# Kernel tuning notes

Measured on AMD Instinct MI355X. Metric: run time of the kernel, lower is better.

## Reference

```python
import jax, jax.numpy as jnp
import numpy as np

B, S, D, H = 2, 2048, 1024, 16
HD = D // H               # head_dim = input_size / num_heads
STEPS = 1                 # update_steps_max extra Hopfield update steps
LN_EPS = 1e-5
SCALING = 1.0 / np.sqrt(HD)  # beta = 1/sqrt(head_dim)


def layernorm(x, g, b):
    m = x.mean(-1, keepdims=True)
    v = ((x - m) ** 2).mean(-1, keepdims=True)
    return (x - m) * jax.lax.rsqrt(v + LN_EPS) * g + b


def setup_inputs() -> dict:
    key = jax.random.key(0)
    ks = jax.random.split(key, 9)
    s = 0.02
    f32 = jnp.float32
    return {
        "data": jax.random.normal(ks[0], (B, S, D), f32),
        # affine LayerNorm params (stored / state / projection patterns)
        "g_k": jnp.ones((D,), f32), "b_k": jnp.zeros((D,), f32),
        "g_q": jnp.ones((D,), f32), "b_q": jnp.zeros((D,), f32),
        "g_v": jnp.ones((D,), f32), "b_v": jnp.zeros((D,), f32),
        # in-projections (q/k/v) and out-projection of HopfieldCore
        "Wq": jax.random.normal(ks[1], (D, D), f32) * s, "bq": jnp.zeros((D,), f32),
        "Wk": jax.random.normal(ks[2], (D, D), f32) * s, "bk": jnp.zeros((D,), f32),
        "Wv": jax.random.normal(ks[3], (D, D), f32) * s, "bv": jnp.zeros((D,), f32),
        "Wo": jax.random.normal(ks[4], (D, D), f32) * s, "bo": jnp.zeros((D,), f32),
    }


def reference(data, g_k, b_k, g_q, b_q, g_v, b_v,
              Wq, bq, Wk, bk, Wv, bv, Wo, bo):
    # single input tensor used as stored / state / projection pattern
    xk = layernorm(data, g_k, b_k)   # stored pattern  -> keys
    xq = layernorm(data, g_q, b_q)   # state pattern   -> queries
    xv = layernorm(data, g_v, b_v)   # pattern proj    -> values

    split = lambda t: t.reshape(B, S, H, HD).transpose(0, 2, 1, 3)  # [B,H,S,HD]
    q = split(xq @ Wq + bq)
    k = split(xk @ Wk + bk)
    v = split(xv @ Wv + bv)

    def assoc(q):  # xi = softmax(beta * q K^T)
        return jax.nn.softmax(
            jnp.einsum('bhqd,bhkd->bhqk', q, k) * SCALING, axis=-1)

    xi = assoc(q)
    for _ in range(STEPS):           # iterative Hopfield update: q <- xi K
        q = jnp.einsum('bhqk,bhkd->bhqd', xi, k)
        xi = assoc(q)

    out = jnp.einsum('bhqk,bhkd->bhqd', xi, v)        # retrieve with values
    out = out.transpose(0, 2, 1, 3).reshape(B, S, D)  # merge heads
    return out @ Wo + bo
```

## Files before the change

### kernel.cpp

```cpp
#include <hip/hip_runtime.h>
#include <hip/hip_bf16.h>

#define B_  2
#define S_  2048
#define D_  1024
#define H_  16
#define HD_ 64
#define M_  4096


typedef __attribute__((ext_vector_type(8))) short short8;
typedef __attribute__((ext_vector_type(4))) float f32x4;
typedef __attribute__((ext_vector_type(2))) float f32x2;
typedef __attribute__((ext_vector_type(16))) float f32x16;

#define CE_ 0.1803368801111204f

typedef __attribute__((address_space(1))) const unsigned GU;
typedef __attribute__((address_space(3))) unsigned LU;
static __device__ __forceinline__ void glds16(const void* g, void* l){
  __builtin_amdgcn_global_load_lds((GU*)g, (LU*)l, 16, 0, 0);
}

static __device__ __forceinline__ unsigned short f2bfc(float f){
  union{float f; unsigned u;} c; c.f = f;
  return (unsigned short)((c.u + 0x8000u) >> 16);
}
static __device__ __forceinline__ unsigned pk2bf(float a, float b){
  union{float f; unsigned u;} ca, cb; ca.f=a; cb.f=b;
  return __builtin_amdgcn_perm(cb.u + 0x8000u, ca.u + 0x8000u, 0x07060302u);
}
static __device__ __forceinline__ unsigned pk2bft(float a, float b){
  union{float f; unsigned u;} ca, cb; ca.f=a; cb.f=b;
  return __builtin_amdgcn_perm(cb.u, ca.u, 0x07060302u);
}
static __device__ __forceinline__ short8 mk8(unsigned x0, unsigned x1,
                                             unsigned x2, unsigned x3){
  union{ unsigned u[4]; short8 s; } t;
  t.u[0]=x0; t.u[1]=x1; t.u[2]=x2; t.u[3]=x3; return t.s;
}
static __device__ __forceinline__ void plswap(unsigned &x, unsigned &y){
  auto r = __builtin_amdgcn_permlane32_swap(x, y, false, false);
  x = (unsigned)r[0]; y = (unsigned)r[1];
}
static __device__ __forceinline__ short8 conv8a(const f32x16& v, float iv){
  unsigned a0 = pk2bf(v[0]*iv, v[1]*iv);
  unsigned a1 = pk2bf(v[2]*iv, v[3]*iv);
  unsigned b0 = pk2bf(v[4]*iv, v[5]*iv);
  unsigned b1 = pk2bf(v[6]*iv, v[7]*iv);
  plswap(a0,b0); plswap(a1,b1);
  return mk8(a0,a1,b0,b1);
}
static __device__ __forceinline__ short8 conv8b(const f32x16& v, float iv){
  unsigned a0 = pk2bf(v[8]*iv,  v[9]*iv);
  unsigned a1 = pk2bf(v[10]*iv, v[11]*iv);
  unsigned b0 = pk2bf(v[12]*iv, v[13]*iv);
  unsigned b1 = pk2bf(v[14]*iv, v[15]*iv);
  plswap(a0,b0); plswap(a1,b1);
  return mk8(a0,a1,b0,b1);
}

__global__ __launch_bounds__(256) void prep_kernel(
  const float* __restrict__ data,
  const float* __restrict__ Wq, const float* __restrict__ Wk,
  const float* __restrict__ Wv, const float* __restrict__ Wo,
  const float* __restrict__ gq, const float* __restrict__ gk, const float* __restrict__ gv,
  const float* __restrict__ blq, const float* __restrict__ blk, const float* __restrict__ blv,
  const float* __restrict__ bpq, const float* __restrict__ bpk, const float* __restrict__ bpv,
  unsigned short* __restrict__ WT, unsigned short* __restrict__ xhat,
  float* __restrict__ bf)
{
  __shared__ unsigned short tile[64][72];
  __shared__ float red[4][64];
  int bid = blockIdx.x, t = threadIdx.x;
  if (bid < 1024){
    int z = bid >> 8, rem = bid & 255;
    int k0 = (rem>>4)*64, n0 = (rem&15)*64;
    const float* W = (z==0)?Wq:(z==1)?Wk:(z==2)?Wv:Wo;
    const float* g = (z==0)?gq:(z==1)?gk:(z==2)?gv:(const float*)0;
    unsigned short* out = WT + ((size_t)z<<20);
    {
      int kr = t>>2, c16 = (t&3)*16;
      float gs = g ? g[k0+kr]*((z==0)?CE_:1.0f) : 1.0f;
      const float* src = W + (size_t)(k0+kr)*D_ + n0 + c16;
      float4 w0 = *(const float4*)(src);
      float4 w1 = *(const float4*)(src+4);
      float4 w2 = *(const float4*)(src+8);
      float4 w3 = *(const float4*)(src+12);
      unsigned* tp = (unsigned*)&tile[kr][c16];
      tp[0]=pk2bf(w0.x*gs,w0.y*gs); tp[1]=pk2bf(w0.z*gs,w0.w*gs);
      tp[2]=pk2bf(w1.x*gs,w1.y*gs); tp[3]=pk2bf(w1.z*gs,w1.w*gs);
      tp[4]=pk2bf(w2.x*gs,w2.y*gs); tp[5]=pk2bf(w2.z*gs,w2.w*gs);
      tp[6]=pk2bf(w3.x*gs,w3.y*gs); tp[7]=pk2bf(w3.z*gs,w3.w*gs);
    }
    __syncthreads();
    {
      int nr = t>>2, kc = (t&3)*16;
      union { uint4 v[2]; unsigned short u[16]; } st;
      #pragma unroll
      for (int i=0;i<16;i++) st.u[i] = tile[kc+i][nr];
      unsigned short* dst = out + (size_t)(n0+nr)*D_ + k0 + kc;
      *(uint4*)(dst)     = st.v[0];
      *(uint4*)(dst + 8) = st.v[1];
    }
  } else if (bid < 2048){
    int row = (bid-1024)*4 + (t>>6);
    int l = t & 63;
    const float4* xr = (const float4*)(data + (size_t)row*D_);
    float4 v[4];
    float s = 0.f, ss = 0.f;
    #pragma unroll
    for (int i=0;i<4;i++){
      v[i] = xr[l + 64*i];
      s  += v[i].x+v[i].y+v[i].z+v[i].w;
      ss += v[i].x*v[i].x+v[i].y*v[i].y+v[i].z*v[i].z+v[i].w*v[i].w;
    }
    #pragma unroll
    for (int m=1;m<64;m<<=1){ s += __shfl_xor(s, m, 64); ss += __shfl_xor(ss, m, 64); }
    float me = s*(1.0f/D_);
    float var = ss*(1.0f/D_) - me*me;
    float rs = rsqrtf(var + 1e-5f);
    float nm = -me*rs;
    unsigned short* xo = xhat + (size_t)row*D_;
    #pragma unroll
    for (int i=0;i<4;i++){
      uint2 pk;
      pk.x = pk2bf(fmaf(v[i].x,rs,nm), fmaf(v[i].y,rs,nm));
      pk.y = pk2bf(fmaf(v[i].z,rs,nm), fmaf(v[i].w,rs,nm));
      *(uint2*)(xo + 4*l + 256*i) = pk;
    }
  } else {
    int idx = bid - 2048;
    int z = idx >> 4, xb = idx & 15;
    const float* W  = (z==0)?Wq:(z==1)?Wk:Wv;
    const float* bl = (z==0)?blq:(z==1)?blk:blv;
    const float* bp = (z==0)?bpq:(z==1)?bpk:bpv;
    int nl = t & 63, kg = t >> 6;
    int n = xb*64 + nl;
    float acc = 0.f;
    for (int k = kg*256; k < (kg+1)*256; k++)
      acc += bl[k] * W[(size_t)k*D_ + n];
    red[kg][nl] = acc;
    __syncthreads();
    if (t < 64){
      int nn = xb*64 + t;
      float v = red[0][t]+red[1][t]+red[2][t]+red[3][t] + bp[nn];
      bf[z*D_ + nn] = (z==0) ? v*CE_ : v;
    }
  }
}

__global__ __launch_bounds__(256) void gemm_qkv(
  const unsigned short* __restrict__ xhat,
  const unsigned short* __restrict__ WT,
  const float* __restrict__ biasf,
  unsigned short* __restrict__ qv, unsigned short* __restrict__ kb,
  unsigned short* __restrict__ kT, unsigned short* __restrict__ vT)
{
  int z = blockIdx.z;
  const unsigned short* Bt = WT + ((size_t)z<<20);
  const float* bias = biasf + z*D_;
  unsigned short* oN = (z==0)?qv:(z==1)?kb:(unsigned short*)0;
  unsigned short* oT = (z==0)?(unsigned short*)0:(z==1)?kT:vT;

  __shared__ __align__(16) unsigned short As[128*32];
  __shared__ __align__(16) unsigned short Bs[128*32];
  int tid = threadIdx.x, w = tid>>6, l = tid&63;
  int m0 = blockIdx.x*128, n0 = blockIdx.y*128;
  int wr = (w>>1)*64, wc = (w&1)*64;
  int lr = l&15, qd = l>>4;

  const unsigned short* gA = xhat + (size_t)(m0 + w*32 + (l>>2))*D_ + (l&3)*8;
  const unsigned short* gB = Bt   + (size_t)(n0 + w*32 + (l>>2))*D_ + (l&3)*8;
  unsigned short* lA0 = &As[(w*32)*32];
  unsigned short* lA1 = &As[(w*32+16)*32];
  unsigned short* lB0 = &Bs[(w*32)*32];
  unsigned short* lB1 = &Bs[(w*32+16)*32];

  const f32x4 fz = {0.f,0.f,0.f,0.f};
  f32x4 acc[4][4];
  #pragma unroll
  for (int i=0;i<4;i++)
    #pragma unroll
    for (int j=0;j<4;j++) acc[i][j] = fz;

  for (int kk=0; kk<D_; kk+=32){
    __syncthreads();
    glds16(gA + kk,                 lA0);
    glds16(gA + kk + (size_t)16*D_, lA1);
    glds16(gB + kk,                 lB0);
    glds16(gB + kk + (size_t)16*D_, lB1);
    __syncthreads();
    short8 af[4], bfr[4];
    #pragma unroll
    for (int i=0;i<4;i++) af[i]  = *(const short8*)(As + (wr + i*16 + lr)*32 + qd*8);
    #pragma unroll
    for (int j=0;j<4;j++) bfr[j] = *(const short8*)(Bs + (wc + j*16 + lr)*32 + qd*8);
    #pragma unroll
    for (int i=0;i<4;i++)
      #pragma unroll
      for (int j=0;j<4;j++)
        acc[i][j] = __builtin_amdgcn_mfma_f32_16x16x32_bf16(af[i], bfr[j], acc[i][j], 0, 0, 0);
  }

  #pragma unroll
  for (int j=0;j<4;j++){
    int n = n0 + wc + j*16 + lr;
    float bias_n = bias[n];
    #pragma unroll
    for (int i=0;i<4;i++){
      int mb = m0 + wr + i*16 + qd*4;
      float v0 = acc[i][j][0] + bias_n;
      float v1 = acc[i][j][1] + bias_n;
      float v2 = acc[i][j][2] + bias_n;
      float v3 = acc[i][j][3] + bias_n;
      if (oN){
        oN[(size_t)(mb+0)*D_ + n] = f2bfc(v0);
        oN[(size_t)(mb+1)*D_ + n] = f2bfc(v1);
        oN[(size_t)(mb+2)*D_ + n] = f2bfc(v2);
        oN[(size_t)(mb+3)*D_ + n] = f2bfc(v3);
      }
      if (oT){
        int bb = mb >> 11, sI = mb & (S_-1);
        int hh = n >> 6,  dd = n & 63;
        uint2 pk; pk.x = pk2bf(v0, v1); pk.y = pk2bf(v2, v3);
        *(uint2*)(oT + (size_t)((bb*H_ + hh)*HD_ + dd)*S_ + sI) = pk;
      }
    }
  }
}

__global__ __launch_bounds__(256) void gemm_out(
  const unsigned short* __restrict__ A,
  const unsigned short* __restrict__ Bt,
  const float* __restrict__ bo,
  float* __restrict__ Cf)
{
  __shared__ __align__(16) unsigned short As[128*32];
  __shared__ __align__(16) unsigned short Bs[128*32];
  int tid = threadIdx.x, w = tid>>6, l = tid&63;
  int m0 = blockIdx.x*128, n0 = blockIdx.y*128;
  int wr = (w>>1)*64, wc = (w&1)*64;
  int lr = l&15, qd = l>>4;

  const unsigned short* gA = A  + (size_t)(m0 + w*32 + (l>>2))*D_ + (l&3)*8;
  const unsigned short* gB = Bt + (size_t)(n0 + w*32 + (l>>2))*D_ + (l&3)*8;
  unsigned short* lA0 = &As[(w*32)*32];
  unsigned short* lA1 = &As[(w*32+16)*32];
  unsigned short* lB0 = &Bs[(w*32)*32];
  unsigned short* lB1 = &Bs[(w*32+16)*32];

  const f32x4 fz = {0.f,0.f,0.f,0.f};
  f32x4 acc[4][4];
  #pragma unroll
  for (int i=0;i<4;i++)
    #pragma unroll
    for (int j=0;j<4;j++) acc[i][j] = fz;

  for (int kk=0; kk<D_; kk+=32){
    __syncthreads();
    glds16(gA + kk,                 lA0);
    glds16(gA + kk + (size_t)16*D_, lA1);
    glds16(gB + kk,                 lB0);
    glds16(gB + kk + (size_t)16*D_, lB1);
    __syncthreads();
    short8 af[4], bfr[4];
    #pragma unroll
    for (int i=0;i<4;i++) af[i]  = *(const short8*)(As + (wr + i*16 + lr)*32 + qd*8);
    #pragma unroll
    for (int j=0;j<4;j++) bfr[j] = *(const short8*)(Bs + (wc + j*16 + lr)*32 + qd*8);
    #pragma unroll
    for (int i=0;i<4;i++)
      #pragma unroll
      for (int j=0;j<4;j++)
        acc[i][j] = __builtin_amdgcn_mfma_f32_16x16x32_bf16(af[i], bfr[j], acc[i][j], 0, 0, 0);
  }

  #pragma unroll
  for (int j=0;j<4;j++){
    int n = n0 + wc + j*16 + lr;
    float bias_n = bo[n];
    #pragma unroll
    for (int i=0;i<4;i++){
      int mb = m0 + wr + i*16 + qd*4;
      Cf[(size_t)(mb+0)*D_ + n] = acc[i][j][0] + bias_n;
      Cf[(size_t)(mb+1)*D_ + n] = acc[i][j][1] + bias_n;
      Cf[(size_t)(mb+2)*D_ + n] = acc[i][j][2] + bias_n;
      Cf[(size_t)(mb+3)*D_ + n] = acc[i][j][3] + bias_n;
    }
  }
}

__global__ __launch_bounds__(256, 4) void attn_fused(
  unsigned short* __restrict__ QO,
  const unsigned short* __restrict__ K,
  const unsigned short* __restrict__ KT,
  const unsigned short* __restrict__ VT)
{
  int qt = blockIdx.x;
  int h  = blockIdx.y;
  int b  = qt >> 5;
  int bh = b*H_ + h;
  int tid = threadIdx.x, w = tid>>6, l = tid&63;
  int wq = w & 1, wk = w >> 1;
  int lq = l & 31, hi = l >> 5;
  int swzr = (lq & 7) << 3;

  __shared__ __align__(16) unsigned short smem[17408];

  const f32x16 fz16 = {0.f,0.f,0.f,0.f,0.f,0.f,0.f,0.f,
                       0.f,0.f,0.f,0.f,0.f,0.f,0.f,0.f};

  const unsigned short* Qb = QO + (size_t)(qt*64 + wq*32 + lq)*D_ + h*64;
  short8 qf[4];
  #pragma unroll
  for (int d=0; d<4; d++) qf[d] = *(const short8*)(Qb + d*16 + hi*8);

  const unsigned short* Khead = K + (size_t)(b*S_)*D_ + h*64;
  const unsigned short* Vh0 = KT + (size_t)bh*HD_*S_;
  const unsigned short* Vh1 = VT + (size_t)bh*HD_*S_;

  int seg0 = w*2;
  int lr8 = l>>3;
  int swzs = ((l&7)*8) ^ (lr8*8);
  const unsigned short* gKs  = Khead + (size_t)(seg0*8 + lr8)*D_ + swzs;
  const unsigned short* gV0s = Vh0 + (size_t)(seg0*8 + lr8)*S_ + swzs;
  const unsigned short* gV1s = Vh1 + (size_t)(seg0*8 + lr8)*S_ + swzs;
  int dK0 = seg0*512 + l*8;
  int dV0 = 4096 + seg0*512 + l*8;

  glds16(gKs,         smem + dK0);
  glds16(gKs + 8*D_,  smem + dK0 + 512);
  glds16(gV0s,        smem + dV0);
  glds16(gV0s + 8*S_, smem + dV0 + 512);
  __syncthreads();

  #pragma unroll 1
  for (int phase=0; phase<2; phase++){
    f32x16 oacc[2]; oacc[0]=fz16; oacc[1]=fz16;
    f32x2 dq = {0.f,0.f};

    #pragma unroll 1
    for (int ss=0; ss<32; ss++){
      int t = phase*32 + ss;
      if (t < 63){
        int tn = t + 1;
        int tt = tn & 31;
        unsigned short* bb = smem + ((tn&1) ? 8192 : 0);
        const unsigned short* gk = gKs + (size_t)tt*64*D_;
        const unsigned short* gv = ((tn >= 32) ? gV1s : gV0s) + tt*64;
        glds16(gk,         bb + dK0);
        glds16(gk + 8*D_,  bb + dK0 + 512);
        glds16(gv,         bb + dV0);
        glds16(gv + 8*S_,  bb + dV0 + 512);
      }
      __builtin_amdgcn_sched_barrier(0);

      const unsigned short* sKc = smem + ((t&1) ? 8192 : 0);
      const unsigned short* sVc = sKc + 4096;

      f32x16 sc = fz16;
      __builtin_amdgcn_s_setprio(1);
      #pragma unroll
      for (int d4=0; d4<4; d4++){
        short8 ka = *(const short8*)(sKc + (size_t)(wk*32 + lq)*64 + ((d4*16 + hi*8) ^ swzr));
        sc = __builtin_amdgcn_mfma_f32_32x32x16_bf16(ka, qf[d4], sc, 0,0,0);
      }
      __builtin_amdgcn_s_setprio(0);

      #pragma unroll
      for (int i=0;i<16;i++) sc[i] = __builtin_amdgcn_exp2f(sc[i]);
      #pragma unroll
      for (int i=0;i<16;i+=2) dq += (f32x2){sc[i], sc[i+1]};

      short8 pf[2];
      {
        unsigned a0,a1,b0,b1;
        a0=pk2bft(sc[0],sc[1]);   a1=pk2bft(sc[2],sc[3]);
        b0=pk2bft(sc[4],sc[5]);   b1=pk2bft(sc[6],sc[7]);
        plswap(a0,b0); plswap(a1,b1);
        pf[0] = mk8(a0,a1,b0,b1);
        a0=pk2bft(sc[8],sc[9]);   a1=pk2bft(sc[10],sc[11]);
        b0=pk2bft(sc[12],sc[13]); b1=pk2bft(sc[14],sc[15]);
        plswap(a0,b0); plswap(a1,b1);
        pf[1] = mk8(a0,a1,b0,b1);
      }

      __builtin_amdgcn_s_setprio(1);
      #pragma unroll
      for (int dr=0; dr<2; dr++){
        #pragma unroll
        for (int ks=0; ks<2; ks++){
          short8 va = *(const short8*)(sVc + (size_t)(dr*32 + lq)*64 + ((wk*32 + ks*16 + hi*8) ^ swzr));
          oacc[dr] = __builtin_amdgcn_mfma_f32_32x32x16_bf16(va, pf[ks], oacc[dr], 0,0,0);
        }
      }
      __builtin_amdgcn_s_setprio(0);

      __syncthreads();
    }

    float den = dq.x + dq.y;
    den += __shfl_xor(den, 32, 64);

    float* fb  = (float*)(smem + 8192);
    float* dnp = (float*)(smem + 16384);
    if (wk==1){
      #pragma unroll
      for (int dr=0; dr<2; dr++)
        #pragma unroll
        for (int g=0; g<16; g++)
          fb[wq*2048 + (dr*16+g)*64 + l] = oacc[dr][g];
      dnp[wq*64 + l] = den;
    }
    __syncthreads();
    if (wk==0){
      #pragma unroll
      for (int dr=0; dr<2; dr++)
        #pragma unroll
        for (int g=0; g<16; g++)
          oacc[dr][g] += fb[wq*2048 + (dr*16+g)*64 + l];
      den += dnp[wq*64 + l];
      if (phase==0){
        float iv = CE_ * __builtin_amdgcn_rcpf(den);
        qf[0] = conv8a(oacc[0], iv);
        qf[1] = conv8b(oacc[0], iv);
        qf[2] = conv8a(oacc[1], iv);
        qf[3] = conv8b(oacc[1], iv);
        unsigned short* qsh = smem + 8192 + wq*6144;
        #pragma unroll
        for (int d=0; d<4; d++)
          *(short8*)(qsh + d*512 + l*8) = qf[d];
      } else {
        float iv = __builtin_amdgcn_rcpf(den);
        unsigned short* Ob = QO + (size_t)(qt*64 + wq*32 + lq)*D_ + h*64 + hi*4;
        #pragma unroll
        for (int g=0; g<4; g++){
          uint2 pk;
          pk.x = pk2bf(oacc[0][4*g+0]*iv, oacc[0][4*g+1]*iv);
          pk.y = pk2bf(oacc[0][4*g+2]*iv, oacc[0][4*g+3]*iv);
          *(uint2*)(Ob + g*8) = pk;
          pk.x = pk2bf(oacc[1][4*g+0]*iv, oacc[1][4*g+1]*iv);
          pk.y = pk2bf(oacc[1][4*g+2]*iv, oacc[1][4*g+3]*iv);
          *(uint2*)(Ob + 32 + g*8) = pk;
        }
      }
    }
    __syncthreads();
    if (phase==0 && wk==1){
      unsigned short* qsh = smem + 8192 + wq*6144;
      #pragma unroll
      for (int d=0; d<4; d++)
        qf[d] = *(const short8*)(qsh + d*512 + l*8);
    }
    __syncthreads();
  }
}

extern "C" void kernel_launch(void* const* d_in, const int* in_sizes, int n_in,
                              void* d_out, int out_size, void* d_ws, size_t ws_size,
                              hipStream_t stream){
  const float* data = (const float*)d_in[0];
  const float* g_k  = (const float*)d_in[1];
  const float* b_k  = (const float*)d_in[2];
  const float* g_q  = (const float*)d_in[3];
  const float* b_q  = (const float*)d_in[4];
  const float* g_v  = (const float*)d_in[5];
  const float* b_v  = (const float*)d_in[6];
  const float* Wq   = (const float*)d_in[7];
  const float* bq   = (const float*)d_in[8];
  const float* Wk   = (const float*)d_in[9];
  const float* bk   = (const float*)d_in[10];
  const float* Wv   = (const float*)d_in[11];
  const float* bv   = (const float*)d_in[12];
  const float* Wo   = (const float*)d_in[13];
  const float* bo   = (const float*)d_in[14];
  float* out = (float*)d_out;

  char* ws = (char*)d_ws;
  const size_t MB = (size_t)1<<20;
  unsigned short* q    = (unsigned short*)(ws);
  unsigned short* kb   = (unsigned short*)(ws + 8*MB);
  unsigned short* WT   = (unsigned short*)(ws + 16*MB);
  unsigned short* WTo  = WT + ((size_t)3<<20);
  unsigned short* xhat = (unsigned short*)(ws + 24*MB);
  float*          bfld = (float*)(ws + 32*MB);
  unsigned short* vT   = (unsigned short*)d_out;
  unsigned short* kT   = (unsigned short*)((char*)d_out + 8*MB);

  dim3 gb(256);
  prep_kernel<<<dim3(2096), gb, 0, stream>>>(data,
                                             Wq, Wk, Wv, Wo, g_q, g_k, g_v,
                                             b_q, b_k, b_v, bq, bk, bv,
                                             WT, xhat, bfld);
  gemm_qkv<<<dim3(32,8,3), gb, 0, stream>>>(xhat, WT, bfld, q, kb, kT, vT);
  attn_fused<<<dim3(64, H_), gb, 0, stream>>>(q, kb, kT, vT);
  gemm_out<<<dim3(32,8), gb, 0, stream>>>(q, WTo, bo, out);
}
```

Baseline: 254.6 us.

## Halve attention block to two waves, each covering both query halves

The fused attention kernel now runs with 128 threads (2 waves) instead of 256. Each wave computes both 32-row query chunks against its own 32-key slice, so every K/V fragment read from shared memory feeds two MFMAs instead of one. Each wave issues four async global-to-LDS loads per tile instead of two. Block indices are also remapped so consecutive blocks are spread across heads and query tiles. This cuts LDS read traffic per MFMA and the partial-sum exchange, but doubles register pressure per wave and halves waves per block, which may reduce latency hiding.

```diff
diff --git a/kernel.cpp b/kernel.cpp
--- a/kernel.cpp
+++ b/kernel.cpp
@@ -291,54 +291,60 @@
   }
 }
 
-__global__ __launch_bounds__(256, 4) void attn_fused(
+__global__ __launch_bounds__(128, 2) void attn_fused(
   unsigned short* __restrict__ QO,
   const unsigned short* __restrict__ K,
   const unsigned short* __restrict__ KT,
   const unsigned short* __restrict__ VT)
 {
-  int qt = blockIdx.x;
-  int h  = blockIdx.y;
+  int lin = blockIdx.x + (blockIdx.y << 6);
+  int id  = ((lin & 7) << 7) + (lin >> 3);
+  int qt = id & 63;
+  int h  = id >> 6;
   int b  = qt >> 5;
   int bh = b*H_ + h;
   int tid = threadIdx.x, w = tid>>6, l = tid&63;
-  int wq = w & 1, wk = w >> 1;
   int lq = l & 31, hi = l >> 5;
   int swzr = (lq & 7) << 3;
 
-  __shared__ __align__(16) unsigned short smem[17408];
+  __shared__ __align__(16) unsigned short smem[16640];
+  float* dnp = (float*)(smem + 16384);
 
   const f32x16 fz16 = {0.f,0.f,0.f,0.f,0.f,0.f,0.f,0.f,
                        0.f,0.f,0.f,0.f,0.f,0.f,0.f,0.f};
 
-  const unsigned short* Qb = QO + (size_t)(qt*64 + wq*32 + lq)*D_ + h*64;
-  short8 qf[4];
+  const unsigned short* Qb = QO + (size_t)(qt*64 + lq)*D_ + h*64;
+  short8 qf[2][4];
   #pragma unroll
-  for (int d=0; d<4; d++) qf[d] = *(const short8*)(Qb + d*16 + hi*8);
+  for (int qc=0; qc<2; qc++)
+    #pragma unroll
+    for (int d=0; d<4; d++)
+      qf[qc][d] = *(const short8*)(Qb + (size_t)qc*32*D_ + d*16 + hi*8);
 
   const unsigned short* Khead = K + (size_t)(b*S_)*D_ + h*64;
   const unsigned short* Vh0 = KT + (size_t)bh*HD_*S_;
   const unsigned short* Vh1 = VT + (size_t)bh*HD_*S_;
 
-  int seg0 = w*2;
   int lr8 = l>>3;
   int swzs = ((l&7)*8) ^ (lr8*8);
-  const unsigned short* gKs  = Khead + (size_t)(seg0*8 + lr8)*D_ + swzs;
-  const unsigned short* gV0s = Vh0 + (size_t)(seg0*8 + lr8)*S_ + swzs;
-  const unsigned short* gV1s = Vh1 + (size_t)(seg0*8 + lr8)*S_ + swzs;
-  int dK0 = seg0*512 + l*8;
-  int dV0 = 4096 + seg0*512 + l*8;
-
-  glds16(gKs,         smem + dK0);
-  glds16(gKs + 8*D_,  smem + dK0 + 512);
-  glds16(gV0s,        smem + dV0);
-  glds16(gV0s + 8*S_, smem + dV0 + 512);
+  const unsigned short* gKs  = Khead + (size_t)(w*32 + lr8)*D_ + swzs;
+  const unsigned short* gV0s = Vh0 + (size_t)(w*32 + lr8)*S_ + swzs;
+  const unsigned short* gV1s = Vh1 + (size_t)(w*32 + lr8)*S_ + swzs;
+  int dK = w*2048 + l*8;
+  int dV = 4096 + w*2048 + l*8;
+
+  #pragma unroll
+  for (int j=0;j<4;j++){
+    glds16(gKs  + (size_t)j*8*D_, smem + dK + j*512);
+    glds16(gV0s + (size_t)j*8*S_, smem + dV + j*512);
+  }
   __syncthreads();
 
   #pragma unroll 1
   for (int phase=0; phase<2; phase++){
-    f32x16 oacc[2]; oacc[0]=fz16; oacc[1]=fz16;
-    f32x2 dq = {0.f,0.f};
+    f32x16 oacc[2][2];
+    oacc[0][0]=fz16; oacc[0][1]=fz16; oacc[1][0]=fz16; oacc[1][1]=fz16;
+    f32x2 dq0 = {0.f,0.f}, dq1 = {0.f,0.f};
 
     #pragma unroll 1
     for (int ss=0; ss<32; ss++){
@@ -349,41 +355,57 @@
         unsigned short* bb = smem + ((tn&1) ? 8192 : 0);
         const unsigned short* gk = gKs + (size_t)tt*64*D_;
         const unsigned short* gv = ((tn >= 32) ? gV1s : gV0s) + tt*64;
-        glds16(gk,         bb + dK0);
-        glds16(gk + 8*D_,  bb + dK0 + 512);
-        glds16(gv,         bb + dV0);
-        glds16(gv + 8*S_,  bb + dV0 + 512);
+        #pragma unroll
+        for (int j=0;j<4;j++){
+          glds16(gk + (size_t)j*8*D_, bb + dK + j*512);
+          glds16(gv + (size_t)j*8*S_, bb + dV + j*512);
+        }
       }
       __builtin_amdgcn_sched_barrier(0);
 
       const unsigned short* sKc = smem + ((t&1) ? 8192 : 0);
       const unsigned short* sVc = sKc + 4096;
 
-      f32x16 sc = fz16;
+      f32x16 sc0 = fz16, sc1 = fz16;
       __builtin_amdgcn_s_setprio(1);
       #pragma unroll
       for (int d4=0; d4<4; d4++){
-        short8 ka = *(const short8*)(sKc + (size_t)(wk*32 + lq)*64 + ((d4*16 + hi*8) ^ swzr));
-        sc = __builtin_amdgcn_mfma_f32_32x32x16_bf16(ka, qf[d4], sc, 0,0,0);
+        short8 ka = *(const short8*)(sKc + (size_t)(w*32 + lq)*64 + ((d4*16 + hi*8) ^ swzr));
+        sc0 = __builtin_amdgcn_mfma_f32_32x32x16_bf16(ka, qf[0][d4], sc0, 0,0,0);
+        sc1 = __builtin_amdgcn_mfma_f32_32x32x16_bf16(ka, qf[1][d4], sc1, 0,0,0);
       }
       __builtin_amdgcn_s_setprio(0);
 
       #pragma unroll
-      for (int i=0;i<16;i++) sc[i] = __builtin_amdgcn_exp2f(sc[i]);
-      #pragma unroll
-      for (int i=0;i<16;i+=2) dq += (f32x2){sc[i], sc[i+1]};
-
-      short8 pf[2];
+      for (int i=0;i<16;i++){
+        sc0[i] = __builtin_amdgcn_exp2f(sc0[i]);
+        sc1[i] = __builtin_amdgcn_exp2f(sc1[i]);
+      }
+      #pragma unroll
+      for (int i=0;i<16;i+=2){
+        dq0 += (f32x2){sc0[i], sc0[i+1]};
+        dq1 += (f32x2){sc1[i], sc1[i+1]};
+      }
+
+      short8 pf0[2], pf1[2];
       {
         unsigned a0,a1,b0,b1;
-        a0=pk2bft(sc[0],sc[1]);   a1=pk2bft(sc[2],sc[3]);
-        b0=pk2bft(sc[4],sc[5]);   b1=pk2bft(sc[6],sc[7]);
+        a0=pk2bft(sc0[0],sc0[1]);   a1=pk2bft(sc0[2],sc0[3]);
+        b0=pk2bft(sc0[4],sc0[5]);   b1=pk2bft(sc0[6],sc0[7]);
         plswap(a0,b0); plswap(a1,b1);
-        pf[0] = mk8(a0,a1,b0,b1);
-        a0=pk2bft(sc[8],sc[9]);   a1=pk2bft(sc[10],sc[11]);
-        b0=pk2bft(sc[12],sc[13]); b1=pk2bft(sc[14],sc[15]);
+        pf0[0] = mk8(a0,a1,b0,b1);
+        a0=pk2bft(sc0[8],sc0[9]);   a1=pk2bft(sc0[10],sc0[11]);
+        b0=pk2bft(sc0[12],sc0[13]); b1=pk2bft(sc0[14],sc0[15]);
         plswap(a0,b0); plswap(a1,b1);
-        pf[1] = mk8(a0,a1,b0,b1);
+        pf0[1] = mk8(a0,a1,b0,b1);
+        a0=pk2bft(sc1[0],sc1[1]);   a1=pk2bft(sc1[2],sc1[3]);
+        b0=pk2bft(sc1[4],sc1[5]);   b1=pk2bft(sc1[6],sc1[7]);
+        plswap(a0,b0); plswap(a1,b1);
+        pf1[0] = mk8(a0,a1,b0,b1);
+        a0=pk2bft(sc1[8],sc1[9]);   a1=pk2bft(sc1[10],sc1[11]);
+        b0=pk2bft(sc1[12],sc1[13]); b1=pk2bft(sc1[14],sc1[15]);
+        plswap(a0,b0); plswap(a1,b1);
+        pf1[1] = mk8(a0,a1,b0,b1);
       }
 
       __builtin_amdgcn_s_setprio(1);
@@ -391,8 +413,9 @@
       for (int dr=0; dr<2; dr++){
         #pragma unroll
         for (int ks=0; ks<2; ks++){
-          short8 va = *(const short8*)(sVc + (size_t)(dr*32 + lq)*64 + ((wk*32 + ks*16 + hi*8) ^ swzr));
-          oacc[dr] = __builtin_amdgcn_mfma_f32_32x32x16_bf16(va, pf[ks], oacc[dr], 0,0,0);
+          short8 va = *(const short8*)(sVc + (size_t)(dr*32 + lq)*64 + ((w*32 + ks*16 + hi*8) ^ swzr));
+          oacc[0][dr] = __builtin_amdgcn_mfma_f32_32x32x16_bf16(va, pf0[ks], oacc[0][dr], 0,0,0);
+          oacc[1][dr] = __builtin_amdgcn_mfma_f32_32x32x16_bf16(va, pf1[ks], oacc[1][dr], 0,0,0);
         }
       }
       __builtin_amdgcn_s_setprio(0);
@@ -400,58 +423,77 @@
       __syncthreads();
     }
 
-    float den = dq.x + dq.y;
-    den += __shfl_xor(den, 32, 64);
-
-    float* fb  = (float*)(smem + 8192);
-    float* dnp = (float*)(smem + 16384);
-    if (wk==1){
-      #pragma unroll
-      for (int dr=0; dr<2; dr++)
-        #pragma unroll
-        for (int g=0; g<16; g++)
-          fb[wq*2048 + (dr*16+g)*64 + l] = oacc[dr][g];
-      dnp[wq*64 + l] = den;
-    }
-    __syncthreads();
-    if (wk==0){
-      #pragma unroll
-      for (int dr=0; dr<2; dr++)
-        #pragma unroll
-        for (int g=0; g<16; g++)
-          oacc[dr][g] += fb[wq*2048 + (dr*16+g)*64 + l];
-      den += dnp[wq*64 + l];
+    float den0 = dq0.x + dq0.y; den0 += __shfl_xor(den0, 32, 64);
+    float den1 = dq1.x + dq1.y; den1 += __shfl_xor(den1, 32, 64);
+
+    float* fb = (float*)(smem + 8192);
+    if (w==1){
+      #pragma unroll
+      for (int qc=0; qc<2; qc++)
+        #pragma unroll
+        for (int dr=0; dr<2; dr++)
+          #pragma unroll
+          for (int g=0; g<16; g++)
+            fb[(qc*32 + dr*16 + g)*64 + l] = oacc[qc][dr][g];
+      dnp[l]      = den0;
+      dnp[64 + l] = den1;
+    }
+    __syncthreads();
+    if (w==0){
+      #pragma unroll
+      for (int qc=0; qc<2; qc++)
+        #pragma unroll
+        for (int dr=0; dr<2; dr++)
+          #pragma unroll
+          for (int g=0; g<16; g++)
+            oacc[qc][dr][g] += fb[(qc*32 + dr*16 + g)*64 + l];
+      den0 += dnp[l];
+      den1 += dnp[64 + l];
       if (phase==0){
-        float iv = CE_ * __builtin_amdgcn_rcpf(den);
-        qf[0] = conv8a(oacc[0], iv);
-        qf[1] = conv8b(oacc[0], iv);
-        qf[2] = conv8a(oacc[1], iv);
-        qf[3] = conv8b(oacc[1], iv);
-        unsigned short* qsh = smem + 8192 + wq*6144;
+        float iv0 = CE_ * __builtin_amdgcn_rcpf(den0);
+        float iv1 = CE_ * __builtin_amdgcn_rcpf(den1);
+        qf[0][0] = conv8a(oacc[0][0], iv0);
+        qf[0][1] = conv8b(oacc[0][0], iv0);
+        qf[0][2] = conv8a(oacc[0][1], iv0);
+        qf[0][3] = conv8b(oacc[0][1], iv0);
+        qf[1][0] = conv8a(oacc[1][0], iv1);
+        qf[1][1] = conv8b(oacc[1][0], iv1);
+        qf[1][2] = conv8a(oacc[1][1], iv1);
+        qf[1][3] = conv8b(oacc[1][1], iv1);
+        unsigned short* qsh = smem + 8192;
+        #pragma unroll
+        for (int qc=0; qc<2; qc++)
+          #pragma unroll
+          for (int d=0; d<4; d++)
+            *(short8*)(qsh + (size_t)(qc*4 + d)*512 + l*8) = qf[qc][d];
+      } else {
+        float iv0 = __builtin_amdgcn_rcpf(den0);
+        float iv1 = __builtin_amdgcn_rcpf(den1);
+        #pragma unroll
+        for (int qc=0; qc<2; qc++){
+          float iv = qc ? iv1 : iv0;
+          unsigned short* Ob = QO + (size_t)(qt*64 + qc*32 + lq)*D_ + h*64 + hi*4;
+          #pragma unroll
+          for (int g=0; g<4; g++){
+            uint2 pk;
+            pk.x = pk2bf(oacc[qc][0][4*g+0]*iv, oacc[qc][0][4*g+1]*iv);
+            pk.y = pk2bf(oacc[qc][0][4*g+2]*iv, oacc[qc][0][4*g+3]*iv);
+            *(uint2*)(Ob + g*8) = pk;
+            pk.x = pk2bf(oacc[qc][1][4*g+0]*iv, oacc[qc][1][4*g+1]*iv);
+            pk.y = pk2bf(oacc[qc][1][4*g+2]*iv, oacc[qc][1][4*g+3]*iv);
+            *(uint2*)(Ob + 32 + g*8) = pk;
+          }
+        }
+      }
+    }
+    __syncthreads();
+    if (phase==0 && w==1){
+      unsigned short* qsh = smem + 8192;
+      #pragma unroll
+      for (int qc=0; qc<2; qc++)
         #pragma unroll
         for (int d=0; d<4; d++)
-          *(short8*)(qsh + d*512 + l*8) = qf[d];
-      } else {
-        float iv = __builtin_amdgcn_rcpf(den);
-        unsigned short* Ob = QO + (size_t)(qt*64 + wq*32 + lq)*D_ + h*64 + hi*4;
-        #pragma unroll
-        for (int g=0; g<4; g++){
-          uint2 pk;
-          pk.x = pk2bf(oacc[0][4*g+0]*iv, oacc[0][4*g+1]*iv);
-          pk.y = pk2bf(oacc[0][4*g+2]*iv, oacc[0][4*g+3]*iv);
-          *(uint2*)(Ob + g*8) = pk;
-          pk.x = pk2bf(oacc[1][4*g+0]*iv, oacc[1][4*g+1]*iv);
-          pk.y = pk2bf(oacc[1][4*g+2]*iv, oacc[1][4*g+3]*iv);
-          *(uint2*)(Ob + 32 + g*8) = pk;
-        }
-      }
-    }
-    __syncthreads();
-    if (phase==0 && wk==1){
-      unsigned short* qsh = smem + 8192 + wq*6144;
-      #pragma unroll
-      for (int d=0; d<4; d++)
-        qf[d] = *(const short8*)(qsh + d*512 + l*8);
+          qf[qc][d] = *(const short8*)(qsh + (size_t)(qc*4 + d)*512 + l*8);
     }
     __syncthreads();
   }
@@ -494,6 +536,6 @@
                                              b_q, b_k, b_v, bq, bk, bv,
                                              WT, xhat, bfld);
   gemm_qkv<<<dim3(32,8,3), gb, 0, stream>>>(xhat, WT, bfld, q, kb, kT, vT);
-  attn_fused<<<dim3(64, H_), gb, 0, stream>>>(q, kb, kT, vT);
+  attn_fused<<<dim3(64, H_), dim3(128), 0, stream>>>(q, kb, kT, vT);
   gemm_out<<<dim3(32,8), gb, 0, stream>>>(q, WTo, bo, out);
 }
```

New measurement: 242.9 us. 1.05x faster.

## Stage transposed QKV epilogue through LDS and remap attention block order

Applied to the files above, without the earlier changes.

The transposed K/V output of the QKV GEMM is now staged through shared memory, so each thread writes 16-byte contiguous rows along the sequence instead of scattered 8-byte stores. The GEMM's shared buffer is enlarged to hold the padded 128x136 tile, which may lower occupancy. The attention kernel also remaps its linear block index so that consecutive blocks are spread across heads, likely to balance K/V reads across XCD caches.

```diff
diff --git a/kernel.cpp b/kernel.cpp
--- a/kernel.cpp
+++ b/kernel.cpp
@@ -163,8 +163,9 @@
   unsigned short* oN = (z==0)?qv:(z==1)?kb:(unsigned short*)0;
   unsigned short* oT = (z==0)?(unsigned short*)0:(z==1)?kT:vT;
 
-  __shared__ __align__(16) unsigned short As[128*32];
-  __shared__ __align__(16) unsigned short Bs[128*32];
+  __shared__ __align__(16) unsigned short smem[17408];
+  unsigned short* As = smem;
+  unsigned short* Bs = smem + 4096;
   int tid = threadIdx.x, w = tid>>6, l = tid&63;
   int m0 = blockIdx.x*128, n0 = blockIdx.y*128;
   int wr = (w>>1)*64, wc = (w&1)*64;
@@ -203,29 +204,48 @@
         acc[i][j] = __builtin_amdgcn_mfma_f32_16x16x32_bf16(af[i], bfr[j], acc[i][j], 0, 0, 0);
   }
 
-  #pragma unroll
-  for (int j=0;j<4;j++){
-    int n = n0 + wc + j*16 + lr;
-    float bias_n = bias[n];
-    #pragma unroll
-    for (int i=0;i<4;i++){
-      int mb = m0 + wr + i*16 + qd*4;
-      float v0 = acc[i][j][0] + bias_n;
-      float v1 = acc[i][j][1] + bias_n;
-      float v2 = acc[i][j][2] + bias_n;
-      float v3 = acc[i][j][3] + bias_n;
-      if (oN){
-        oN[(size_t)(mb+0)*D_ + n] = f2bfc(v0);
-        oN[(size_t)(mb+1)*D_ + n] = f2bfc(v1);
-        oN[(size_t)(mb+2)*D_ + n] = f2bfc(v2);
-        oN[(size_t)(mb+3)*D_ + n] = f2bfc(v3);
-      }
-      if (oT){
-        int bb = mb >> 11, sI = mb & (S_-1);
-        int hh = n >> 6,  dd = n & 63;
-        uint2 pk; pk.x = pk2bf(v0, v1); pk.y = pk2bf(v2, v3);
-        *(uint2*)(oT + (size_t)((bb*H_ + hh)*HD_ + dd)*S_ + sI) = pk;
-      }
+  if (oN){
+    #pragma unroll
+    for (int j=0;j<4;j++){
+      int n = n0 + wc + j*16 + lr;
+      float bias_n = bias[n];
+      #pragma unroll
+      for (int i=0;i<4;i++){
+        int mb = m0 + wr + i*16 + qd*4;
+        oN[(size_t)(mb+0)*D_ + n] = f2bfc(acc[i][j][0] + bias_n);
+        oN[(size_t)(mb+1)*D_ + n] = f2bfc(acc[i][j][1] + bias_n);
+        oN[(size_t)(mb+2)*D_ + n] = f2bfc(acc[i][j][2] + bias_n);
+        oN[(size_t)(mb+3)*D_ + n] = f2bfc(acc[i][j][3] + bias_n);
+      }
+    }
+  }
+  if (oT){
+    __syncthreads();
+    #pragma unroll
+    for (int j=0;j<4;j++){
+      int nl_ = wc + j*16 + lr;
+      float bias_n = bias[n0 + nl_];
+      #pragma unroll
+      for (int i=0;i<4;i++){
+        int ml_ = wr + i*16 + qd*4;
+        uint2 pk;
+        pk.x = pk2bf(acc[i][j][0] + bias_n, acc[i][j][1] + bias_n);
+        pk.y = pk2bf(acc[i][j][2] + bias_n, acc[i][j][3] + bias_n);
+        *(uint2*)(smem + nl_*136 + ml_) = pk;
+      }
+    }
+    __syncthreads();
+    int bb = m0 >> 11;
+    int s0 = m0 & (S_-1);
+    int dl = tid >> 4;
+    int ml = (tid & 15) * 8;
+    #pragma unroll
+    for (int p=0;p<8;p++){
+      int nl_ = p*16 + dl;
+      int n = n0 + nl_;
+      int hh = n >> 6, dd = n & 63;
+      uint4 vv = *(const uint4*)(smem + nl_*136 + ml);
+      *(uint4*)(oT + (size_t)((bb*H_ + hh)*HD_ + dd)*S_ + (s0 + ml)) = vv;
     }
   }
 }
@@ -297,8 +317,10 @@
   const unsigned short* __restrict__ KT,
   const unsigned short* __restrict__ VT)
 {
-  int qt = blockIdx.x;
-  int h  = blockIdx.y;
+  int lin = blockIdx.x + (blockIdx.y << 6);
+  int id  = ((lin & 7) << 7) + (lin >> 3);
+  int qt = id & 63;
+  int h  = id >> 6;
   int b  = qt >> 5;
   int bh = b*H_ + h;
   int tid = threadIdx.x, w = tid>>6, l = tid&63;
```

Result: no change. 257.9 us (+1.3%).
